# Optimization experiments

Hardware: AMD Instinct MI355X
Metric: run time of the kernel (lower is better)

## Reference

```python
import jax, jax.numpy as jnp
import numpy as np

D_MODEL = 1024
N_HEADS = 16
HEAD_DIM = D_MODEL // N_HEADS
MAX_LEN = 2048
BATCH = 2
SEQ = 2048


def setup_inputs() -> dict:
    key = jax.random.key(0)
    ks = jax.random.split(key, 6)
    std = 1.0 / np.sqrt(D_MODEL)
    x = jax.random.normal(ks[0], (BATCH, SEQ, D_MODEL), dtype=jnp.float32)
    Wqkv = jax.random.uniform(ks[1], (D_MODEL, 3 * D_MODEL), minval=-std, maxval=std, dtype=jnp.float32)
    bqkv = jax.random.uniform(ks[2], (3 * D_MODEL,), minval=-std, maxval=std, dtype=jnp.float32)
    Wout = jax.random.uniform(ks[3], (D_MODEL, D_MODEL), minval=-std, maxval=std, dtype=jnp.float32)
    bout = jax.random.uniform(ks[4], (D_MODEL,), minval=-std, maxval=std, dtype=jnp.float32)
    rel_pos_bias = 0.02 * jax.random.normal(ks[5], (2 * MAX_LEN - 1,), dtype=jnp.float32)
    return {"x": x, "Wqkv": Wqkv, "bqkv": bqkv, "Wout": Wout, "bout": bout, "rel_pos_bias": rel_pos_bias}


def reference(x, Wqkv, bqkv, Wout, bout, rel_pos_bias):
    B, S, _ = x.shape
    scale = HEAD_DIM ** -0.5
    qkv = x @ Wqkv + bqkv                       # [B,S,3*dm]
    qkv = qkv.reshape(B, S, 3, N_HEADS, HEAD_DIM)
    qkv = jnp.transpose(qkv, (2, 0, 3, 1, 4))   # [3,B,H,S,D]
    q, k, v = qkv[0], qkv[1], qkv[2]
    scores = jnp.einsum('bhqd,bhkd->bhqk', q, k) * scale
    pos = jnp.arange(S)
    rel = jnp.clip(pos[:, None] - pos[None, :] + (MAX_LEN - 1), 0, 2 * MAX_LEN - 2)
    scores = scores + rel_pos_bias[rel][None, None]  # bias shared over batch & heads
    probs = jax.nn.softmax(scores, axis=-1)
    out = jnp.einsum('bhqk,bhkd->bhqd', probs, v)    # [B,H,S,D]
    out = jnp.transpose(out, (0, 2, 1, 3)).reshape(B, S, D_MODEL)
    return out @ Wout + bout
```

## Files before the change

### kernel.cpp

```cpp
#include <hip/hip_runtime.h>
#include <cmath>

#define B_ 2
#define S_ 2048
#define H_ 16
#define D_ 64
#define DM 1024

typedef unsigned short u16;
using short8 = __attribute__((ext_vector_type(8))) short;
using f32x4  = __attribute__((ext_vector_type(4))) float;
using f32x16 = __attribute__((ext_vector_type(16))) float;
using i32x4  = __attribute__((ext_vector_type(4))) int;

__device__ __forceinline__ u16 f32_to_bf16(float f) {
    unsigned int u = __float_as_uint(f);
    u += 0x7fffu + ((u >> 16) & 1u);
    return (u16)(u >> 16);
}

__device__ __forceinline__ float exp2_fast(float x) {
    float r;
    asm("v_exp_f32 %0, %1" : "=v"(r) : "v"(x));
    return r;
}

__device__ __forceinline__ int cvt_pk_bf16(float lo, float hi) {
    int r;
    asm("v_cvt_pk_bf16_f32 %0, %1, %2" : "=v"(r) : "v"(lo), "v"(hi));
    return r;
}

__device__ __forceinline__ void gl_lds16(const void* src, void* dst) {
    __builtin_amdgcn_global_load_lds(
        (const __attribute__((address_space(1))) unsigned int*)src,
        (__attribute__((address_space(3))) unsigned int*)dst, 16, 0, 0);
}

__device__ __forceinline__ f32x16 mfma32(short8 a, short8 b, f32x16 c) {
    return __builtin_amdgcn_mfma_f32_32x32x16_bf16(a, b, c, 0, 0, 0);
}

__global__ __launch_bounds__(256) void relattn_prep(
    const float* __restrict__ x, const float* __restrict__ Wqkv,
    const float* __restrict__ Wout, const float* __restrict__ relb,
    u16* __restrict__ xb, u16* __restrict__ WqkvT, u16* __restrict__ WoutT,
    float* __restrict__ relb2)
{
    __shared__ float T[64][65];
    const int tid = threadIdx.x;
    int blk = blockIdx.x;
    if (blk >= 3072) {
        int i0 = ((blk - 3072) * 256 + tid) * 4;
#pragma unroll
        for (int j = 0; j < 4; ++j)
            if (i0 + j < 2 * 2048 - 1)
                relb2[i0 + j] = relb[i0 + j] * 1.44269504f;
        return;
    }
    if (blk < 2048) {
        size_t base = ((size_t)blk * 256 + tid) * 8;
        float4 v0 = *(const float4*)(x + base);
        float4 v1 = *(const float4*)(x + base + 4);
        ushort4 p0 = make_ushort4(f32_to_bf16(v0.x), f32_to_bf16(v0.y),
                                  f32_to_bf16(v0.z), f32_to_bf16(v0.w));
        ushort4 p1 = make_ushort4(f32_to_bf16(v1.x), f32_to_bf16(v1.y),
                                  f32_to_bf16(v1.z), f32_to_bf16(v1.w));
        *(ushort4*)(xb + base) = p0;
        *(ushort4*)(xb + base + 4) = p1;
        return;
    }
    int id = blk - 2048;
    const float* in; u16* outp; int R, C;
    if (id < 768) { in = Wqkv; outp = WqkvT; R = 1024; C = 3072; }
    else          { id -= 768; in = Wout;  outp = WoutT; R = 1024; C = 1024; }
    const int tpr = C >> 6;
    const int r0 = (id / tpr) << 6, c0 = (id % tpr) << 6;
#pragma unroll
    for (int it = 0; it < 4; ++it) {
        int e = tid + it * 256;
        int row = e >> 4, c4 = (e & 15) << 2;
        float4 v = *(const float4*)(in + (size_t)(r0 + row) * C + c0 + c4);
        T[row][c4 + 0] = v.x; T[row][c4 + 1] = v.y;
        T[row][c4 + 2] = v.z; T[row][c4 + 3] = v.w;
    }
    __syncthreads();
#pragma unroll
    for (int it = 0; it < 4; ++it) {
        int e = tid + it * 256;
        int crow = e >> 4, r4 = (e & 15) << 2;
        ushort4 pk = make_ushort4(f32_to_bf16(T[r4 + 0][crow]), f32_to_bf16(T[r4 + 1][crow]),
                                  f32_to_bf16(T[r4 + 2][crow]), f32_to_bf16(T[r4 + 3][crow]));
        *(ushort4*)(outp + (size_t)(c0 + crow) * R + r0 + r4) = pk;
    }
}

__global__ __launch_bounds__(256) void relattn_gemm_qkv(
    const u16* __restrict__ A, const u16* __restrict__ Bm,
    const float* __restrict__ bias, u16* __restrict__ qk, u16* __restrict__ Vt)
{
    __shared__ alignas(16) unsigned char AsB[16384];
    __shared__ alignas(16) unsigned char BsB[16384];
    const int tid = threadIdx.x;
    const int w = tid >> 6, l = tid & 63, ln = l & 15, hi = l >> 4;
    const int wr = w >> 1, wc = w & 1;
    const int row0 = blockIdx.y * 128, col0 = blockIdx.x * 128;
    const char* Ab = (const char*)A;
    const char* Bb = (const char*)Bm;

    f32x4 acc[4][4] = {};
    for (int step = 0; step < 16; ++step) {
        __syncthreads();
#pragma unroll
        for (int it = 0; it < 4; ++it) {
            int dsto = it * 4096 + w * 1024;
            int o = dsto + l * 16;
            int row = o >> 7;
            int swz = (o & 127) ^ ((row & 7) << 4);
            gl_lds16(Ab + (size_t)(row0 + row) * 2048 + step * 128 + swz, AsB + dsto);
            gl_lds16(Bb + (size_t)(col0 + row) * 2048 + step * 128 + swz, BsB + dsto);
        }
        __syncthreads();
#pragma unroll
        for (int kk = 0; kk < 2; ++kk) {
            short8 a[4], b[4];
            const int kb = hi * 16 + kk * 64;
#pragma unroll
            for (int m = 0; m < 4; ++m) {
                int row = wr * 64 + m * 16 + ln;
                a[m] = *(const short8*)(AsB + row * 128 + (kb ^ ((row & 7) << 4)));
            }
#pragma unroll
            for (int n = 0; n < 4; ++n) {
                int row = wc * 64 + n * 16 + ln;
                b[n] = *(const short8*)(BsB + row * 128 + (kb ^ ((row & 7) << 4)));
            }
#pragma unroll
            for (int m = 0; m < 4; ++m)
#pragma unroll
                for (int n = 0; n < 4; ++n)
                    acc[m][n] = __builtin_amdgcn_mfma_f32_16x16x32_bf16(a[m], b[n], acc[m][n], 0, 0, 0);
        }
    }

    const int t = col0 >> 10;
    const int bb = row0 >> 11;
    if (t < 2) {
#pragma unroll
        for (int n = 0; n < 4; ++n) {
            int c = col0 + wc * 64 + n * 16 + ln;
            int h = (c >> 6) & 15, d = c & 63;
            float bv = bias[c];
            u16* plane = qk + (size_t)((t * B_ + bb) * H_ + h) * S_ * D_;
#pragma unroll
            for (int m = 0; m < 4; ++m)
#pragma unroll
                for (int r = 0; r < 4; ++r) {
                    int s = (row0 + wr * 64 + m * 16 + hi * 4 + r) & (S_ - 1);
                    plane[(size_t)s * D_ + d] = f32_to_bf16(acc[m][n][r] + bv);
                }
        }
    } else {
#pragma unroll
        for (int n = 0; n < 4; ++n) {
            int c = col0 + wc * 64 + n * 16 + ln;
            int h = (c >> 6) & 15, d = c & 63;
            float bv = bias[c];
            u16* vrow = Vt + (size_t)((bb * H_ + h) * D_ + d) * S_;
#pragma unroll
            for (int m = 0; m < 4; ++m) {
                int s = (row0 + wr * 64 + m * 16 + hi * 4) & (S_ - 1);
                ushort4 pk = make_ushort4(f32_to_bf16(acc[m][n][0] + bv),
                                          f32_to_bf16(acc[m][n][1] + bv),
                                          f32_to_bf16(acc[m][n][2] + bv),
                                          f32_to_bf16(acc[m][n][3] + bv));
                *(ushort4*)(vrow + s) = pk;
            }
        }
    }
}

__global__ __launch_bounds__(256) void relattn_attn(
    const u16* __restrict__ qk, const u16* __restrict__ Vt,
    const float* __restrict__ relb2, u16* __restrict__ aout)
{
    __shared__ alignas(16) unsigned char Lds[32768];
    const int tid = threadIdx.x;
    const int w = tid >> 6, l = tid & 63;
    const int l31 = l & 31, h2 = l >> 5;
    const int qt = blockIdx.x, bh = blockIdx.y;
    const int bb = bh >> 4;
    const char* qpl = (const char*)(qk + (size_t)bh * (S_ * D_));
    const char* kpl = (const char*)(qk + (size_t)(B_ * H_ + bh) * (S_ * D_));
    const char* vpl = (const char*)(Vt + (size_t)bh * (D_ * S_));

    const int q0 = qt * 128 + w * 32;
    const int qrow = q0 + l31;

    short8 qf[4];
#pragma unroll
    for (int kd = 0; kd < 4; ++kd)
        qf[kd] = *(const short8*)(qpl + (size_t)qrow * 128 + kd * 32 + h2 * 16);

    f32x16 O0 = {}, O1 = {};
    float mrun = -1e30f, lrun = 0.f;

    {
#pragma unroll
        for (int it = 0; it < 2; ++it) {
            int dsto = it * 4096 + w * 1024;
            int o = dsto + l * 16;
            int row = o >> 7;
            int swz = (o & 127) ^ ((row & 7) << 4);
            gl_lds16(kpl + (size_t)row * 128 + swz, Lds + dsto);
            gl_lds16(vpl + (size_t)row * (S_ * 2) + swz, Lds + 8192 + dsto);
        }
    }
    __syncthreads();

    for (int kt = 0; kt < S_ / 64; ++kt) {
        const int buf = kt & 1;
        const unsigned char* KB = Lds + buf * 16384;
        const unsigned char* VB = KB + 8192;

        if (kt < S_ / 64 - 1) {
#pragma unroll
            for (int it = 0; it < 2; ++it) {
                int dsto = it * 4096 + w * 1024;
                int o = dsto + l * 16;
                int row = o >> 7;
                int swz = (o & 127) ^ ((row & 7) << 4);
                unsigned char* db = Lds + (buf ^ 1) * 16384 + dsto;
                gl_lds16(kpl + (size_t)((kt + 1) * 64 + row) * 128 + swz, db);
                gl_lds16(vpl + (size_t)row * (S_ * 2) + (kt + 1) * 128 + swz, db + 8192);
            }
        }

        f32x16 s0 = {}, s1 = {};
#pragma unroll
        for (int kd = 0; kd < 4; ++kd) {
            int kbyte = kd * 32 + h2 * 16;
            int sw = (l31 & 7) << 4;
            short8 k0 = *(const short8*)(KB + l31 * 128 + (kbyte ^ sw));
            short8 k1 = *(const short8*)(KB + (32 + l31) * 128 + (kbyte ^ sw));
            s0 = mfma32(k0, qf[kd], s0);
            s1 = mfma32(k1, qf[kd], s1);
        }

        const float SC2 = 0.125f * 1.44269504f;
        const float* bp = relb2 + (qrow - kt * 64 - 4 * h2 + 2047);
#pragma unroll
        for (int rq = 0; rq < 4; ++rq)
#pragma unroll
            for (int j = 0; j < 4; ++j) {
                s0[rq * 4 + j] = s0[rq * 4 + j] * SC2 + bp[-(8 * rq + j)];
                s1[rq * 4 + j] = s1[rq * 4 + j] * SC2 + bp[-(32 + 8 * rq + j)];
            }

        float tm = -1e30f;
#pragma unroll
        for (int r = 0; r < 16; ++r) {
            tm = fmaxf(tm, s0[r]);
            tm = fmaxf(tm, s1[r]);
        }
        tm = fmaxf(tm, __shfl_xor(tm, 32));
        float nm = fmaxf(mrun, tm);
        float al = exp2_fast(mrun - nm);
        mrun = nm;
        float ps = 0.f;
#pragma unroll
        for (int r = 0; r < 16; ++r) { s0[r] = exp2_fast(s0[r] - nm); ps += s0[r]; }
#pragma unroll
        for (int r = 0; r < 16; ++r) { s1[r] = exp2_fast(s1[r] - nm); ps += s1[r]; }
        ps += __shfl_xor(ps, 32);
        lrun = lrun * al + ps;
#pragma unroll
        for (int r = 0; r < 16; ++r) { O0[r] *= al; O1[r] *= al; }

#pragma unroll
        for (int ts = 0; ts < 4; ++ts) {
            float p0, p1, p2, p3, p4, p5, p6, p7;
            if (ts == 0)      { p0=s0[0];  p1=s0[1];  p2=s0[2];  p3=s0[3];  p4=s0[4];  p5=s0[5];  p6=s0[6];  p7=s0[7]; }
            else if (ts == 1) { p0=s0[8];  p1=s0[9];  p2=s0[10]; p3=s0[11]; p4=s0[12]; p5=s0[13]; p6=s0[14]; p7=s0[15]; }
            else if (ts == 2) { p0=s1[0];  p1=s1[1];  p2=s1[2];  p3=s1[3];  p4=s1[4];  p5=s1[5];  p6=s1[6];  p7=s1[7]; }
            else              { p0=s1[8];  p1=s1[9];  p2=s1[10]; p3=s1[11]; p4=s1[12]; p5=s1[13]; p6=s1[14]; p7=s1[15]; }
            int c01 = cvt_pk_bf16(p0, p1), c23 = cvt_pk_bf16(p2, p3);
            int c45 = cvt_pk_bf16(p4, p5), c67 = cvt_pk_bf16(p6, p7);
            int px01 = __shfl_xor(c01, 32), px23 = __shfl_xor(c23, 32);
            int px45 = __shfl_xor(c45, 32), px67 = __shfl_xor(c67, 32);
            i32x4 pw;
            pw[0] = h2 ? px45 : c01;
            pw[1] = h2 ? px67 : c23;
            pw[2] = h2 ? c45 : px01;
            pw[3] = h2 ? c67 : px23;
            short8 pb = __builtin_bit_cast(short8, pw);
            int vbyte = ts * 32 + h2 * 16;
            int sw = (l31 & 7) << 4;
            short8 v0 = *(const short8*)(VB + l31 * 128 + (vbyte ^ sw));
            short8 v1 = *(const short8*)(VB + (32 + l31) * 128 + (vbyte ^ sw));
            O0 = mfma32(v0, pb, O0);
            O1 = mfma32(v1, pb, O1);
        }
        __syncthreads();
    }

    float inv = 1.0f / lrun;
    u16* orow = aout + (size_t)(bb * S_ + qrow) * DM + (bh & 15) * 64 + 4 * h2;
#pragma unroll
    for (int g = 0; g < 4; ++g) {
        ushort4 w0 = make_ushort4(f32_to_bf16(O0[4 * g + 0] * inv), f32_to_bf16(O0[4 * g + 1] * inv),
                                  f32_to_bf16(O0[4 * g + 2] * inv), f32_to_bf16(O0[4 * g + 3] * inv));
        ushort4 w1 = make_ushort4(f32_to_bf16(O1[4 * g + 0] * inv), f32_to_bf16(O1[4 * g + 1] * inv),
                                  f32_to_bf16(O1[4 * g + 2] * inv), f32_to_bf16(O1[4 * g + 3] * inv));
        *(ushort4*)(orow + 8 * g) = w0;
        *(ushort4*)(orow + 32 + 8 * g) = w1;
    }
}

__global__ __launch_bounds__(256) void relattn_gemm_out(
    const u16* __restrict__ A, const u16* __restrict__ Bm,
    const float* __restrict__ bias, float* __restrict__ out)
{
    __shared__ alignas(16) unsigned char AsB[16384];
    __shared__ alignas(16) unsigned char BsB[16384];
    const int tid = threadIdx.x;
    const int w = tid >> 6, l = tid & 63, ln = l & 15, hi = l >> 4;
    const int wr = w >> 1, wc = w & 1;
    const int row0 = blockIdx.y * 128, col0 = blockIdx.x * 128;
    const char* Ab = (const char*)A;
    const char* Bb = (const char*)Bm;

    f32x4 acc[4][4] = {};
    for (int step = 0; step < 16; ++step) {
        __syncthreads();
#pragma unroll
        for (int it = 0; it < 4; ++it) {
            int dsto = it * 4096 + w * 1024;
            int o = dsto + l * 16;
            int row = o >> 7;
            int swz = (o & 127) ^ ((row & 7) << 4);
            gl_lds16(Ab + (size_t)(row0 + row) * 2048 + step * 128 + swz, AsB + dsto);
            gl_lds16(Bb + (size_t)(col0 + row) * 2048 + step * 128 + swz, BsB + dsto);
        }
        __syncthreads();
#pragma unroll
        for (int kk = 0; kk < 2; ++kk) {
            short8 a[4], b[4];
            const int kb = hi * 16 + kk * 64;
#pragma unroll
            for (int m = 0; m < 4; ++m) {
                int row = wr * 64 + m * 16 + ln;
                a[m] = *(const short8*)(AsB + row * 128 + (kb ^ ((row & 7) << 4)));
            }
#pragma unroll
            for (int n = 0; n < 4; ++n) {
                int row = wc * 64 + n * 16 + ln;
                b[n] = *(const short8*)(BsB + row * 128 + (kb ^ ((row & 7) << 4)));
            }
#pragma unroll
            for (int m = 0; m < 4; ++m)
#pragma unroll
                for (int n = 0; n < 4; ++n)
                    acc[m][n] = __builtin_amdgcn_mfma_f32_16x16x32_bf16(a[m], b[n], acc[m][n], 0, 0, 0);
        }
    }

#pragma unroll
    for (int n = 0; n < 4; ++n) {
        int c = col0 + wc * 64 + n * 16 + ln;
        float bv = bias[c];
#pragma unroll
        for (int m = 0; m < 4; ++m)
#pragma unroll
            for (int r = 0; r < 4; ++r) {
                int row = row0 + wr * 64 + m * 16 + hi * 4 + r;
                out[(size_t)row * DM + c] = acc[m][n][r] + bv;
            }
    }
}

extern "C" void kernel_launch(void* const* d_in, const int* in_sizes, int n_in,
                              void* d_out, int out_size, void* d_ws, size_t ws_size,
                              hipStream_t stream) {
    const float* x    = (const float*)d_in[0];
    const float* Wqkv = (const float*)d_in[1];
    const float* bqkv = (const float*)d_in[2];
    const float* Wout = (const float*)d_in[3];
    const float* bout = (const float*)d_in[4];
    const float* relb = (const float*)d_in[5];
    float* out = (float*)d_out;

    u16* ws    = (u16*)d_ws;
    u16* xb    = ws;
    u16* WqkvT = xb + 4194304;
    u16* WoutT = WqkvT + 3145728;
    u16* qkpl  = WoutT + 1048576;
    u16* Vt    = qkpl + 8388608;
    u16* aout  = Vt + 4194304;
    float* relb2 = (float*)(aout + 4194304);

    relattn_prep<<<3076, 256, 0, stream>>>(x, Wqkv, Wout, relb, xb, WqkvT, WoutT, relb2);
    relattn_gemm_qkv<<<dim3(24, 32), 256, 0, stream>>>(xb, WqkvT, bqkv, qkpl, Vt);
    relattn_attn<<<dim3(16, 32), 256, 0, stream>>>(qkpl, Vt, relb2, aout);
    relattn_gemm_out<<<dim3(8, 32), 256, 0, stream>>>(aout, WoutT, bout, out);
}
```

Before: 146.3 us.

## Split the KV range across two wave groups in attention with an LDS merge

The attention block grows to 512 threads. Two groups of four waves each process half of the key/value sequence for the same 128 queries, each with its own double-buffered LDS region. At the end, the second group writes its partial O, running max and running sum to LDS, and the first group merges them with an online-softmax rescale before writing the output. This is meant to raise resident waves per CU and hide load latency, at the cost of doubled LDS per block, an extra merge step, and a register cap from the new launch bounds.

```diff
diff --git a/kernel.cpp b/kernel.cpp
--- a/kernel.cpp
+++ b/kernel.cpp
@@ -180,22 +180,25 @@
     }
 }
 
-__global__ __launch_bounds__(256) void relattn_attn(
+__global__ __launch_bounds__(512, 4) void relattn_attn(
     const u16* __restrict__ qk, const u16* __restrict__ Vt,
     const float* __restrict__ relb2, u16* __restrict__ aout)
 {
-    __shared__ alignas(16) unsigned char Lds[32768];
+    __shared__ alignas(16) unsigned char Lds[65536];
     const int tid = threadIdx.x;
     const int w = tid >> 6, l = tid & 63;
+    const int wg = w & 3, g = w >> 2;
     const int l31 = l & 31, h2 = l >> 5;
     const int qt = blockIdx.x, bh = blockIdx.y;
     const int bb = bh >> 4;
     const char* qpl = (const char*)(qk + (size_t)bh * (S_ * D_));
     const char* kpl = (const char*)(qk + (size_t)(B_ * H_ + bh) * (S_ * D_));
     const char* vpl = (const char*)(Vt + (size_t)bh * (D_ * S_));
-
-    const int q0 = qt * 128 + w * 32;
+    unsigned char* GB = Lds + g * 32768;
+
+    const int q0 = qt * 128 + wg * 32;
     const int qrow = q0 + l31;
+    const int kvbase = g * 1024;
 
     short8 qf[4];
 #pragma unroll
@@ -208,31 +211,32 @@
     {
 #pragma unroll
         for (int it = 0; it < 2; ++it) {
-            int dsto = it * 4096 + w * 1024;
+            int dsto = it * 4096 + wg * 1024;
             int o = dsto + l * 16;
             int row = o >> 7;
             int swz = (o & 127) ^ ((row & 7) << 4);
-            gl_lds16(kpl + (size_t)row * 128 + swz, Lds + dsto);
-            gl_lds16(vpl + (size_t)row * (S_ * 2) + swz, Lds + 8192 + dsto);
+            gl_lds16(kpl + (size_t)(kvbase + row) * 128 + swz, GB + dsto);
+            gl_lds16(vpl + (size_t)row * (S_ * 2) + kvbase * 2 + swz, GB + 8192 + dsto);
         }
     }
     __syncthreads();
 
-    for (int kt = 0; kt < S_ / 64; ++kt) {
+    for (int kt = 0; kt < 16; ++kt) {
         const int buf = kt & 1;
-        const unsigned char* KB = Lds + buf * 16384;
+        const unsigned char* KB = GB + buf * 16384;
         const unsigned char* VB = KB + 8192;
-
-        if (kt < S_ / 64 - 1) {
+        const int kv0 = kvbase + kt * 64;
+
+        if (kt < 15) {
 #pragma unroll
             for (int it = 0; it < 2; ++it) {
-                int dsto = it * 4096 + w * 1024;
+                int dsto = it * 4096 + wg * 1024;
                 int o = dsto + l * 16;
                 int row = o >> 7;
                 int swz = (o & 127) ^ ((row & 7) << 4);
-                unsigned char* db = Lds + (buf ^ 1) * 16384 + dsto;
-                gl_lds16(kpl + (size_t)((kt + 1) * 64 + row) * 128 + swz, db);
-                gl_lds16(vpl + (size_t)row * (S_ * 2) + (kt + 1) * 128 + swz, db + 8192);
+                unsigned char* db = GB + (buf ^ 1) * 16384 + dsto;
+                gl_lds16(kpl + (size_t)(kv0 + 64 + row) * 128 + swz, db);
+                gl_lds16(vpl + (size_t)row * (S_ * 2) + (kv0 + 64) * 2 + swz, db + 8192);
             }
         }
 
@@ -248,7 +252,7 @@
         }
 
         const float SC2 = 0.125f * 1.44269504f;
-        const float* bp = relb2 + (qrow - kt * 64 - 4 * h2 + 2047);
+        const float* bp = relb2 + (qrow - kv0 - 4 * h2 + 2047);
 #pragma unroll
         for (int rq = 0; rq < 4; ++rq)
 #pragma unroll
@@ -304,16 +308,44 @@
         __syncthreads();
     }
 
-    float inv = 1.0f / lrun;
-    u16* orow = aout + (size_t)(bb * S_ + qrow) * DM + (bh & 15) * 64 + 4 * h2;
-#pragma unroll
-    for (int g = 0; g < 4; ++g) {
-        ushort4 w0 = make_ushort4(f32_to_bf16(O0[4 * g + 0] * inv), f32_to_bf16(O0[4 * g + 1] * inv),
-                                  f32_to_bf16(O0[4 * g + 2] * inv), f32_to_bf16(O0[4 * g + 3] * inv));
-        ushort4 w1 = make_ushort4(f32_to_bf16(O1[4 * g + 0] * inv), f32_to_bf16(O1[4 * g + 1] * inv),
-                                  f32_to_bf16(O1[4 * g + 2] * inv), f32_to_bf16(O1[4 * g + 3] * inv));
-        *(ushort4*)(orow + 8 * g) = w0;
-        *(ushort4*)(orow + 32 + 8 * g) = w1;
+    {
+        float* PO = (float*)(Lds + wg * 8704);
+        float* PM = (float*)(Lds + wg * 8704 + 8192);
+        float* PL = (float*)(Lds + wg * 8704 + 8448);
+        if (g == 1) {
+#pragma unroll
+            for (int r = 0; r < 16; ++r) {
+                PO[l * 32 + r] = O0[r];
+                PO[l * 32 + 16 + r] = O1[r];
+            }
+            PM[l] = mrun;
+            PL[l] = lrun;
+        }
+        __syncthreads();
+        if (g == 1) return;
+        float m1v = PM[l], l1v = PL[l];
+        float nm = fmaxf(mrun, m1v);
+        float a0 = exp2_fast(mrun - nm), a1 = exp2_fast(m1v - nm);
+        float lr = lrun * a0 + l1v * a1;
+        float inv = 1.0f / lr;
+        const float* src = PO + l * 32;
+        u16* orow = aout + (size_t)(bb * S_ + qrow) * DM + (bh & 15) * 64 + 4 * h2;
+#pragma unroll
+        for (int gq = 0; gq < 4; ++gq) {
+            ushort4 w0, w1;
+            float o00 = (O0[4*gq+0] * a0 + src[4*gq+0] * a1) * inv;
+            float o01 = (O0[4*gq+1] * a0 + src[4*gq+1] * a1) * inv;
+            float o02 = (O0[4*gq+2] * a0 + src[4*gq+2] * a1) * inv;
+            float o03 = (O0[4*gq+3] * a0 + src[4*gq+3] * a1) * inv;
+            float o10 = (O1[4*gq+0] * a0 + src[16+4*gq+0] * a1) * inv;
+            float o11 = (O1[4*gq+1] * a0 + src[16+4*gq+1] * a1) * inv;
+            float o12 = (O1[4*gq+2] * a0 + src[16+4*gq+2] * a1) * inv;
+            float o13 = (O1[4*gq+3] * a0 + src[16+4*gq+3] * a1) * inv;
+            w0 = make_ushort4(f32_to_bf16(o00), f32_to_bf16(o01), f32_to_bf16(o02), f32_to_bf16(o03));
+            w1 = make_ushort4(f32_to_bf16(o10), f32_to_bf16(o11), f32_to_bf16(o12), f32_to_bf16(o13));
+            *(ushort4*)(orow + 8 * gq) = w0;
+            *(ushort4*)(orow + 32 + 8 * gq) = w1;
+        }
     }
 }
 
@@ -401,6 +433,6 @@
 
     relattn_prep<<<3076, 256, 0, stream>>>(x, Wqkv, Wout, relb, xb, WqkvT, WoutT, relb2);
     relattn_gemm_qkv<<<dim3(24, 32), 256, 0, stream>>>(xb, WqkvT, bqkv, qkpl, Vt);
-    relattn_attn<<<dim3(16, 32), 256, 0, stream>>>(qkpl, Vt, relb2, aout);
+    relattn_attn<<<dim3(16, 32), 512, 0, stream>>>(qkpl, Vt, relb2, aout);
     relattn_gemm_out<<<dim3(8, 32), 256, 0, stream>>>(aout, WoutT, bout, out);
 }
```

Measured after the change: 138.6 us. -5.3%, faster.
